# Performance work log

Measured on AMD Instinct MI355X. Metric: run time of the kernel, lower is better.

The kernel has to match this reference:

```python
import jax, jax.numpy as jnp
import numpy as np

OUT_C, IN_C, KS, KN = 256, 256, 3, 4
TEMP = 1.0
D1 = OUT_C * KS            # 768
D2 = IN_C * KS             # 768
D2R = D2 // 2 + 1          # 385 (rfft width)


def _freq_indices():
    # mirror torch get_fft2freq(d1, d2, use_rfft=True)
    fh = np.fft.fftfreq(D1)
    fw = np.fft.rfftfreq(D2)
    grid = np.stack(np.meshgrid(fh, fw, indexing='ij'), axis=-1)  # (D1, D2R, 2)
    dist = np.linalg.norm(grid, axis=-1).ravel()
    idx = np.argsort(dist, kind='stable')
    return (idx // D2R).astype(np.int32), (idx % D2R).astype(np.int32)


def setup_inputs() -> dict:
    key = jax.random.key(0)
    k1, k2, k3 = jax.random.split(key, 3)
    b, h, w = 8, 64, 64
    fh, fw = _freq_indices()
    num_freq = fh.shape[0]  # 295680 = D1 * D2R (param_reduction == 1.0)
    return {
        'x': jax.random.normal(k1, (b, IN_C, h, w), dtype=jnp.float32),
        'dft_weight': jax.random.normal(k2, (KN, num_freq, 2), dtype=jnp.float32) * 1e-6,
        'k_att': jax.random.normal(k3, (b, KN, 1, 1), dtype=jnp.float32),
        'freq_h': jnp.asarray(fh),
        'freq_w': jnp.asarray(fw),
    }


def reference(x, dft_weight, k_att, freq_h, freq_w):
    b, c, h, w = x.shape
    # kernel attention: sigmoid(att / temp) * 2 / kernel_num
    att = jax.nn.sigmoid(k_att / TEMP) * (2.0 / KN)          # (b, KN, 1, 1)
    # weighted sum of per-kernel frequency weights -> (b, F, 2)
    wsum = jnp.einsum('knf,bk->bnf', dft_weight, att.reshape(b, KN))
    wc = jax.lax.complex(wsum[..., 0], wsum[..., 1])          # (b, F) complex
    # scatter into dense rfft2 map (indices are a permutation: no duplicates)
    dft_map = jnp.zeros((b, D1, D2R), dtype=jnp.complex64)
    dft_map = dft_map.at[:, freq_h, freq_w].set(wc)
    # inverse rFFT2 -> spatial weights (b, D1, D2)
    sw = jnp.fft.irfft2(dft_map, s=(D1, D2))
    # (b, out, ks, in, ks) -> (b, out, in, ks, ks) -> grouped-conv kernel
    wk = sw.reshape(b, OUT_C, KS, IN_C, KS).transpose(0, 1, 3, 2, 4)
    wk = wk.reshape(b * OUT_C, IN_C, KS, KS)
    # batch of per-sample convs == one grouped conv with groups=b
    xg = x.reshape(1, b * c, h, w)
    out = jax.lax.conv_general_dilated(
        xg, wk, window_strides=(1, 1), padding=[(1, 1), (1, 1)],
        dimension_numbers=('NCHW', 'OIHW', 'NCHW'), feature_group_count=b)
    return out.reshape(b, OUT_C, out.shape[2], out.shape[3])
```

## Files before the change

### kernel.cpp

```cpp
#include <hip/hip_runtime.h>
#include <math.h>

#define D1 768
#define D2R 385
#define NF 295680
#define KNUM 4
#define NB 8
#define NC 256
#define TWOPI_768 0.008181230868723419f
#define INV768 0.0013020833333333333f

#define ATW_U32 1572864u
#define YA_U32 2752512u
#define T_U32 3981312u
#define SPECB_K_U32 344064u
#define WBF_BYTE 9437184u

typedef __attribute__((ext_vector_type(8))) short short8;
typedef __attribute__((ext_vector_type(16))) float f32x16;
typedef __attribute__((ext_vector_type(4))) float f4;
union U4S8 { unsigned int u[4]; uint4 u4; short8 s8; };

static __device__ __forceinline__ unsigned int f2bf(float f) {
  unsigned int u = __float_as_uint(f);
  return (u + 0x7fffu + ((u >> 16) & 1u)) >> 16;
}

static __device__ __forceinline__ void sincos_rev768(int idx, float* s,
                                                     float* c) {
  float rev = (float)idx * INV768;
  *s = __builtin_amdgcn_sinf(rev);
  *c = __builtin_amdgcn_cosf(rev);
}

static __device__ __forceinline__ void barrier_lgkm() {
  asm volatile("s_waitcnt lgkmcnt(0)" ::: "memory");
  __builtin_amdgcn_sched_barrier(0);
  __builtin_amdgcn_s_barrier();
  __builtin_amdgcn_sched_barrier(0);
}

__global__ __launch_bounds__(256) void prep_kernel(
    const float* __restrict__ dw, const int* __restrict__ fh,
    const int* __restrict__ fw, unsigned int* __restrict__ ws) {
  long i = (long)blockIdx.x * 256 + threadIdx.x;
  if (i < 1182720) {
    int k = (int)(i / NF);
    int r = (int)(i - (long)k * NF);
    const float2 v = ((const float2*)dw)[i];
    int h = fh[r], c = fw[r];
    ws[(size_t)k * SPECB_K_U32 + (size_t)c * 768 + h] =
        f2bf(v.x) | (f2bf(v.y) << 16);
    return;
  }
  long j = i - 1182720;
  if (j < 1179648) {
    int ri = (int)(j / 589824);
    int rem = (int)(j - (long)ri * 589824);
    int m = rem / 768, h = rem - (rem / 768) * 768;
    int idx = (h * m) % 768;
    float s, c;
    sincos_rev768(idx, &s, &c);
    unsigned lo, hi;
    if (ri == 0) { lo = f2bf(c); hi = f2bf(-s); }
    else         { lo = f2bf(s); hi = f2bf(c); }
    ws[ATW_U32 + j] = lo | (hi << 16);
  } else if (j < 1486848) {
    long p = j - 1179648;
    int n = (int)(p / 400), cc = (int)(p - (p / 400) * 400);
    unsigned v = 0;
    if (cc <= 384) {
      float wgt = (cc == 0 || cc == 384) ? 1.6954210069444445e-6f
                                         : 3.390842013888889e-6f;
      int idx = (cc * n) % 768;
      float s, c;
      sincos_rev768(idx, &s, &c);
      v = f2bf(wgt * c) | (f2bf(-wgt * s) << 16);
    }
    ws[T_U32 + (size_t)n * 400 + cc] = v;
  } else if (j < 1680384) {
    long p = j - 1486848;
    int k = (int)(p / 48384);
    long r = p - (long)k * 48384;
    int row = 385 + (int)(r / 768);
    int col = (int)(r - (r / 768) * 768);
    ws[(size_t)k * SPECB_K_U32 + (size_t)row * 768 + col] = 0u;
  } else if (j < 1726464) {
    long p = j - 1680384;
    int k = (int)(p / 11520);
    long r = p - (long)k * 11520;
    int m = (int)(r / 15), jj = (int)(r - (r / 15) * 15);
    ws[YA_U32 + (size_t)k * 307200 + (size_t)m * 400 + 385 + jj] = 0u;
  }
}

__global__ __launch_bounds__(256) void fftA_kernel(
    const unsigned short* __restrict__ Atw,
    const unsigned short* __restrict__ specB,
    unsigned short* __restrict__ Ya) {
  __shared__ __align__(16) unsigned short Al[2][64 * 40], Bl[2][64 * 40];
  int t = threadIdx.x;
  int mt = blockIdx.x, nt = blockIdx.y, z = blockIdx.z;
  int ri = z & 1, k = z >> 1;
  const unsigned short* Ag =
      Atw + (size_t)ri * 1179648 + (size_t)(mt * 64) * 1536;
  const unsigned short* Bg =
      specB + (size_t)k * 688128 + (size_t)(nt * 64) * 1536;
  int rowS = t >> 2, q = t & 3;
  int lane = t & 63, w = t >> 6;
  int moff = (w & 1) * 32, noff = (w >> 1) * 32;
  int lm = lane & 31, half = lane >> 5;
  int wr = rowS * 40 + q * 8;
  int ao = (moff + lm) * 40 + half * 8;
  int bo = (noff + lm) * 40 + half * 8;

  f32x16 acc;
#pragma unroll
  for (int r = 0; r < 16; ++r) acc[r] = 0.f;

  uint4 av = *(const uint4*)(Ag + (size_t)rowS * 1536 + q * 8);
  uint4 bv = *(const uint4*)(Bg + (size_t)rowS * 1536 + q * 8);
  *(uint4*)&Al[0][wr] = av;
  *(uint4*)&Bl[0][wr] = bv;
  __syncthreads();

  for (int kb = 0; kb < 48; ++kb) {
    bool more = (kb < 47);
    if (more) {
      av = *(const uint4*)(Ag + (size_t)rowS * 1536 + (kb + 1) * 32 + q * 8);
      bv = *(const uint4*)(Bg + (size_t)rowS * 1536 + (kb + 1) * 32 + q * 8);
    }
    const unsigned short* Ab = Al[kb & 1];
    const unsigned short* Bb = Bl[kb & 1];
#pragma unroll
    for (int kk2 = 0; kk2 < 2; ++kk2) {
      short8 a8 = *(const short8*)&Ab[ao + kk2 * 16];
      short8 b8 = *(const short8*)&Bb[bo + kk2 * 16];
      acc = __builtin_amdgcn_mfma_f32_32x32x16_bf16(a8, b8, acc, 0, 0, 0);
    }
    if (more) {
      *(uint4*)&Al[(kb + 1) & 1][wr] = av;
      *(uint4*)&Bl[(kb + 1) & 1][wr] = bv;
    }
    __syncthreads();
  }

  int c = nt * 64 + noff + lm;
  if (c < D2R) {
    unsigned short* Yk = Ya + (size_t)k * 614400;
    int mb = mt * 64 + moff + 4 * half;
#pragma unroll
    for (int reg = 0; reg < 16; ++reg) {
      int m = mb + (reg & 3) + 8 * (reg >> 2);
      Yk[(size_t)m * 800 + 2 * c + ri] = (unsigned short)f2bf(acc[reg]);
    }
  }
}

__global__ __launch_bounds__(256) void fftB_kernel(
    const unsigned short* __restrict__ Ya, const unsigned short* __restrict__ T,
    float* __restrict__ SW) {
  __shared__ __align__(16) unsigned short Al[2][64 * 40], Bl[2][64 * 40];
  int t = threadIdx.x;
  int mt = blockIdx.x, nt = blockIdx.y, k = blockIdx.z;
  const unsigned short* Ag = Ya + (size_t)k * 614400 + (size_t)(mt * 64) * 800;
  const unsigned short* Bg = T + (size_t)(nt * 64) * 800;
  int rowS = t >> 2, q = t & 3;
  int lane = t & 63, w = t >> 6;
  int moff = (w & 1) * 32, noff = (w >> 1) * 32;
  int lm = lane & 31, half = lane >> 5;
  int wr = rowS * 40 + q * 8;
  int ao = (moff + lm) * 40 + half * 8;
  int bo = (noff + lm) * 40 + half * 8;

  f32x16 acc;
#pragma unroll
  for (int r = 0; r < 16; ++r) acc[r] = 0.f;

  uint4 av = *(const uint4*)(Ag + (size_t)rowS * 800 + q * 8);
  uint4 bv = *(const uint4*)(Bg + (size_t)rowS * 800 + q * 8);
  *(uint4*)&Al[0][wr] = av;
  *(uint4*)&Bl[0][wr] = bv;
  __syncthreads();

  for (int kb = 0; kb < 25; ++kb) {
    bool more = (kb < 24);
    if (more) {
      av = *(const uint4*)(Ag + (size_t)rowS * 800 + (kb + 1) * 32 + q * 8);
      bv = *(const uint4*)(Bg + (size_t)rowS * 800 + (kb + 1) * 32 + q * 8);
    }
    const unsigned short* Ab = Al[kb & 1];
    const unsigned short* Bb = Bl[kb & 1];
#pragma unroll
    for (int kk2 = 0; kk2 < 2; ++kk2) {
      short8 a8 = *(const short8*)&Ab[ao + kk2 * 16];
      short8 b8 = *(const short8*)&Bb[bo + kk2 * 16];
      acc = __builtin_amdgcn_mfma_f32_32x32x16_bf16(a8, b8, acc, 0, 0, 0);
    }
    if (more) {
      *(uint4*)&Al[(kb + 1) & 1][wr] = av;
      *(uint4*)&Bl[(kb + 1) & 1][wr] = bv;
    }
    __syncthreads();
  }

  float* SWk = SW + (size_t)k * 589824;
  int n = nt * 64 + noff + lm;
  int mb = mt * 64 + moff + 4 * half;
#pragma unroll
  for (int reg = 0; reg < 16; ++reg) {
    int m = mb + (reg & 3) + 8 * (reg >> 2);
    SWk[(size_t)m * 768 + n] = acc[reg];
  }
}

__global__ __launch_bounds__(256) void wprep_kernel(
    const float* __restrict__ ka, const float* __restrict__ SW,
    unsigned short* __restrict__ wBF) {
  __shared__ float rowL[4][768];
  int t = threadIdx.x;
  int row = blockIdx.x;
  int oc = row / 3, dy = row - oc * 3;
  if (t < 192) {
#pragma unroll
    for (int k = 0; k < 4; ++k)
      *(float4*)&rowL[k][t * 4] =
          *(const float4*)(SW + (size_t)k * 589824 + (size_t)row * 768 + t * 4);
  }
  float att[8][4];
#pragma unroll
  for (int b = 0; b < 8; ++b)
#pragma unroll
    for (int k = 0; k < 4; ++k)
      att[b][k] = 0.5f / (1.f + expf(-ka[b * 4 + k]));
  __syncthreads();
  int icb = t >> 4, i = t & 15;
#pragma unroll
  for (int dx = 0; dx < 3; ++dx) {
    int col = icb * 48 + dx + 3 * i;
    float v0 = rowL[0][col], v1 = rowL[1][col], v2 = rowL[2][col],
          v3 = rowL[3][col];
    int s = dy * 3 + dx;
#pragma unroll
    for (int b = 0; b < 8; ++b) {
      float v = att[b][0] * v0 + att[b][1] * v1 + att[b][2] * v2 +
                att[b][3] * v3;
      wBF[(((size_t)(b * 16 + icb) * 9 + s) * 256 + oc) * 16 + i] =
          (unsigned short)f2bf(v);
    }
  }
}

static __device__ __forceinline__ void stage_write(unsigned char* xw, f4 v0,
                                                   f4 v1, f4 v2, f4 v3) {
#pragma unroll
  for (int pp = 0; pp < 4; ++pp) {
    uint2 wv;
    wv.x = f2bf(v0[pp]) | (f2bf(v1[pp]) << 16);
    wv.y = f2bf(v2[pp]) | (f2bf(v3[pp]) << 16);
    *(uint2*)(xw + pp * 48) = wv;
  }
}

__global__ __launch_bounds__(256, 2) void conv_mfma_kernel(
    const float* __restrict__ x, const unsigned short* __restrict__ wBF,
    float* __restrict__ out) {
  __shared__ __align__(16) unsigned char ldsX[2][4 * 66 * 48];
  int t = threadIdx.x;
  int pxt = blockIdx.x, oct = blockIdx.y, b = blockIdx.z;
  int py0 = pxt * 2, oc0 = oct * 128;
  int lane = t & 63, w = t >> 6;
  int ocq = w >> 1, pxq = w & 1;
  int n = lane & 31, half = lane >> 5;

  if (t < 192) {
    int buf = t / 96, r2 = t - buf * 96;
    int site = r2 / 12, word = r2 - site * 12;
    int r = site >> 1, c = (site & 1) ? 65 : 0;
    *(unsigned int*)(&ldsX[buf][(r * 66 + c) * 48 + word * 4]) = 0u;
  }

  f32x16 acc[2][2];
#pragma unroll
  for (int i = 0; i < 2; ++i)
#pragma unroll
    for (int j = 0; j < 2; ++j)
#pragma unroll
      for (int r = 0; r < 16; ++r) acc[i][j][r] = 0.f;

  int px4 = lane & 15, sub = lane >> 4;
  int iy = py0 - 1 + sub;
  bool valid = (iy >= 0 && iy < 64);
  const float* xpb =
      x + (((size_t)(b * NC + w * 4)) * 64 + (valid ? iy : 0)) * 64 + px4 * 4;
  int xwbase = (sub * 66 + 1 + px4 * 4) * 48 + w * 8;

  f4 a0 = {0.f, 0.f, 0.f, 0.f}, a1 = a0, a2 = a0, a3 = a0;
  if (valid) {
    const float* p0 = xpb;
    a0 = *(const f4*)(p0);
    a1 = *(const f4*)(p0 + 4096);
    a2 = *(const f4*)(p0 + 8192);
    a3 = *(const f4*)(p0 + 12288);
  }

  const uint4* wg4 = (const uint4*)wBF;
  size_t abase =
      (size_t)b * 144 * 512 + (size_t)(oc0 + ocq * 64 + n) * 2 + half;
  U4S8 pf[9][2];
#pragma unroll
  for (int i = 0; i < 9; ++i) {
    pf[i][0].u4 = wg4[abase + (size_t)i * 512];
    pf[i][1].u4 = wg4[abase + (size_t)i * 512 + 64];
  }

  stage_write(&ldsX[0][0] + xwbase, a0, a1, a2, a3);
  barrier_lgkm();

  for (int icb = 0; icb < 16; ++icb) {
    a0 = a1 = a2 = a3 = (f4){0.f, 0.f, 0.f, 0.f};
    if (icb < 15 && valid) {
      const float* p0 = xpb + (size_t)(icb + 1) * 16 * 4096;
      a0 = *(const f4*)(p0);
      a1 = *(const f4*)(p0 + 4096);
      a2 = *(const f4*)(p0 + 8192);
      a3 = *(const f4*)(p0 + 12288);
    }
    const unsigned char* bufR = &ldsX[icb & 1][0];
#pragma unroll
    for (int s = 0; s < 9; ++s) {
      int step = icb * 9 + s;
      int dy = s / 3, dx = s - dy * 3;
      const unsigned char* bb =
          bufR + ((pxq + dy) * 66 + n + dx) * 48 + half * 16;
      short8 B0 = *(const short8*)bb;
      short8 B1 = *(const short8*)(bb + 32 * 48);
      acc[0][0] = __builtin_amdgcn_mfma_f32_32x32x16_bf16(pf[s][0].s8, B0,
                                                          acc[0][0], 0, 0, 0);
      acc[0][1] = __builtin_amdgcn_mfma_f32_32x32x16_bf16(pf[s][0].s8, B1,
                                                          acc[0][1], 0, 0, 0);
      acc[1][0] = __builtin_amdgcn_mfma_f32_32x32x16_bf16(pf[s][1].s8, B0,
                                                          acc[1][0], 0, 0, 0);
      acc[1][1] = __builtin_amdgcn_mfma_f32_32x32x16_bf16(pf[s][1].s8, B1,
                                                          acc[1][1], 0, 0, 0);
      if (icb < 15) {
        pf[s][0].u4 = wg4[abase + (size_t)(step + 9) * 512];
        pf[s][1].u4 = wg4[abase + (size_t)(step + 9) * 512 + 64];
      }
    }
    if (icb < 15)
      stage_write(&ldsX[(icb + 1) & 1][0] + xwbase, a0, a1, a2, a3);
    barrier_lgkm();
  }

  int py = py0 + pxq;
#pragma unroll
  for (int osub = 0; osub < 2; ++osub)
#pragma unroll
    for (int psub = 0; psub < 2; ++psub) {
      int OC = oc0 + ocq * 64 + osub * 32 + 4 * half;
      int pxc = psub * 32 + n;
      float* op = out + (((size_t)(b * NC + OC)) * 64 + py) * 64 + pxc;
#pragma unroll
      for (int reg = 0; reg < 16; ++reg) {
        int ocm = (reg & 3) + 8 * (reg >> 2);
        op[(size_t)ocm * 4096] = acc[osub][psub][reg];
      }
    }
}

extern "C" void kernel_launch(void* const* d_in, const int* in_sizes, int n_in,
                              void* d_out, int out_size, void* d_ws,
                              size_t ws_size, hipStream_t stream) {
  const float* x = (const float*)d_in[0];
  const float* dw = (const float*)d_in[1];
  const float* ka = (const float*)d_in[2];
  const int* fh = (const int*)d_in[3];
  const int* fw = (const int*)d_in[4];
  float* out = (float*)d_out;
  unsigned int* ws = (unsigned int*)d_ws;
  const unsigned short* specB = (const unsigned short*)d_ws;
  const unsigned short* Atw = (const unsigned short*)((char*)d_ws + 6291456);
  unsigned short* Ya = (unsigned short*)((char*)d_ws + 11010048);
  const unsigned short* T = (const unsigned short*)((char*)d_ws + 15925248);
  float* SW = (float*)d_ws;
  unsigned short* wBF = (unsigned short*)((char*)d_ws + WBF_BYTE);

  hipLaunchKernelGGL(prep_kernel, dim3(11364), dim3(256), 0, stream, dw, fh,
                     fw, ws);
  hipLaunchKernelGGL(fftA_kernel, dim3(12, 7, 8), dim3(256), 0, stream, Atw,
                     specB, Ya);
  hipLaunchKernelGGL(fftB_kernel, dim3(12, 12, KNUM), dim3(256), 0, stream, Ya,
                     T, SW);
  hipLaunchKernelGGL(wprep_kernel, dim3(768), dim3(256), 0, stream, ka, SW,
                     wBF);
  hipLaunchKernelGGL(conv_mfma_kernel, dim3(32, 2, NB), dim3(256), 0, stream,
                     x, wBF, out);
}
```

Before: 192.7 us.

## Enlarge FFT GEMM M-tiles, remap conv blocks per XCD, shrink conv LDS stride

The two DFT GEMM kernels now compute 128x64 tiles per block with two accumulators per wave, so each B fragment read from LDS feeds two MFMAs and half as many blocks are launched. The conv kernel is launched on a 1D grid and remaps block IDs so that blocks sharing a batch and output-channel slice land on the same XCD, which should improve L2 reuse of weights and input. The conv input staging changes to a strided pixel assignment with a 40-byte LDS row stride instead of 48, reducing LDS footprint and changing the bank pattern, at the cost of scalar global loads instead of float4. The larger GEMM tiles reduce block-level parallelism for the small FFT GEMMs and raise register pressure.

```diff
diff --git a/kernel.cpp b/kernel.cpp
--- a/kernel.cpp
+++ b/kernel.cpp
@@ -18,7 +18,6 @@
 
 typedef __attribute__((ext_vector_type(8))) short short8;
 typedef __attribute__((ext_vector_type(16))) float f32x16;
-typedef __attribute__((ext_vector_type(4))) float f4;
 union U4S8 { unsigned int u[4]; uint4 u4; short8 s8; };
 
 static __device__ __forceinline__ unsigned int f2bf(float f) {
@@ -98,61 +97,75 @@
     const unsigned short* __restrict__ Atw,
     const unsigned short* __restrict__ specB,
     unsigned short* __restrict__ Ya) {
-  __shared__ __align__(16) unsigned short Al[2][64 * 40], Bl[2][64 * 40];
+  __shared__ __align__(16) unsigned short Al[2][128 * 40], Bl[2][64 * 40];
   int t = threadIdx.x;
   int mt = blockIdx.x, nt = blockIdx.y, z = blockIdx.z;
   int ri = z & 1, k = z >> 1;
   const unsigned short* Ag =
-      Atw + (size_t)ri * 1179648 + (size_t)(mt * 64) * 1536;
+      Atw + (size_t)ri * 1179648 + (size_t)(mt * 128) * 1536;
   const unsigned short* Bg =
       specB + (size_t)k * 688128 + (size_t)(nt * 64) * 1536;
-  int rowS = t >> 2, q = t & 3;
+  int rowA = t >> 1, qa = t & 1;
+  int rowB = t >> 2, qb = t & 3;
   int lane = t & 63, w = t >> 6;
-  int moff = (w & 1) * 32, noff = (w >> 1) * 32;
+  int mq = w & 1, nq = w >> 1;
   int lm = lane & 31, half = lane >> 5;
-  int wr = rowS * 40 + q * 8;
-  int ao = (moff + lm) * 40 + half * 8;
-  int bo = (noff + lm) * 40 + half * 8;
-
-  f32x16 acc;
-#pragma unroll
-  for (int r = 0; r < 16; ++r) acc[r] = 0.f;
-
-  uint4 av = *(const uint4*)(Ag + (size_t)rowS * 1536 + q * 8);
-  uint4 bv = *(const uint4*)(Bg + (size_t)rowS * 1536 + q * 8);
-  *(uint4*)&Al[0][wr] = av;
-  *(uint4*)&Bl[0][wr] = bv;
+  int wrA = rowA * 40 + qa * 16;
+  int wrB = rowB * 40 + qb * 8;
+  int ao0 = (mq * 64 + lm) * 40 + half * 8;
+  int ao1 = (mq * 64 + 32 + lm) * 40 + half * 8;
+  int bo = (nq * 32 + lm) * 40 + half * 8;
+
+  f32x16 acc[2];
+#pragma unroll
+  for (int i = 0; i < 2; ++i)
+#pragma unroll
+    for (int r = 0; r < 16; ++r) acc[i][r] = 0.f;
+
+  uint4 av0 = *(const uint4*)(Ag + (size_t)rowA * 1536 + qa * 16);
+  uint4 av1 = *(const uint4*)(Ag + (size_t)rowA * 1536 + qa * 16 + 8);
+  uint4 bv = *(const uint4*)(Bg + (size_t)rowB * 1536 + qb * 8);
+  *(uint4*)&Al[0][wrA] = av0;
+  *(uint4*)&Al[0][wrA + 8] = av1;
+  *(uint4*)&Bl[0][wrB] = bv;
   __syncthreads();
 
   for (int kb = 0; kb < 48; ++kb) {
     bool more = (kb < 47);
     if (more) {
-      av = *(const uint4*)(Ag + (size_t)rowS * 1536 + (kb + 1) * 32 + q * 8);
-      bv = *(const uint4*)(Bg + (size_t)rowS * 1536 + (kb + 1) * 32 + q * 8);
+      av0 = *(const uint4*)(Ag + (size_t)rowA * 1536 + (kb + 1) * 32 + qa * 16);
+      av1 = *(const uint4*)(Ag + (size_t)rowA * 1536 + (kb + 1) * 32 + qa * 16 + 8);
+      bv = *(const uint4*)(Bg + (size_t)rowB * 1536 + (kb + 1) * 32 + qb * 8);
     }
     const unsigned short* Ab = Al[kb & 1];
     const unsigned short* Bb = Bl[kb & 1];
 #pragma unroll
     for (int kk2 = 0; kk2 < 2; ++kk2) {
-      short8 a8 = *(const short8*)&Ab[ao + kk2 * 16];
       short8 b8 = *(const short8*)&Bb[bo + kk2 * 16];
-      acc = __builtin_amdgcn_mfma_f32_32x32x16_bf16(a8, b8, acc, 0, 0, 0);
+      short8 a80 = *(const short8*)&Ab[ao0 + kk2 * 16];
+      short8 a81 = *(const short8*)&Ab[ao1 + kk2 * 16];
+      acc[0] = __builtin_amdgcn_mfma_f32_32x32x16_bf16(a80, b8, acc[0], 0, 0, 0);
+      acc[1] = __builtin_amdgcn_mfma_f32_32x32x16_bf16(a81, b8, acc[1], 0, 0, 0);
     }
     if (more) {
-      *(uint4*)&Al[(kb + 1) & 1][wr] = av;
-      *(uint4*)&Bl[(kb + 1) & 1][wr] = bv;
+      *(uint4*)&Al[(kb + 1) & 1][wrA] = av0;
+      *(uint4*)&Al[(kb + 1) & 1][wrA + 8] = av1;
+      *(uint4*)&Bl[(kb + 1) & 1][wrB] = bv;
     }
     __syncthreads();
   }
 
-  int c = nt * 64 + noff + lm;
+  int c = nt * 64 + nq * 32 + lm;
   if (c < D2R) {
     unsigned short* Yk = Ya + (size_t)k * 614400;
-    int mb = mt * 64 + moff + 4 * half;
-#pragma unroll
-    for (int reg = 0; reg < 16; ++reg) {
-      int m = mb + (reg & 3) + 8 * (reg >> 2);
-      Yk[(size_t)m * 800 + 2 * c + ri] = (unsigned short)f2bf(acc[reg]);
+#pragma unroll
+    for (int i = 0; i < 2; ++i) {
+      int mb = mt * 128 + mq * 64 + i * 32 + 4 * half;
+#pragma unroll
+      for (int reg = 0; reg < 16; ++reg) {
+        int m = mb + (reg & 3) + 8 * (reg >> 2);
+        Yk[(size_t)m * 800 + 2 * c + ri] = (unsigned short)f2bf(acc[i][reg]);
+      }
     }
   }
 }
@@ -160,57 +173,71 @@
 __global__ __launch_bounds__(256) void fftB_kernel(
     const unsigned short* __restrict__ Ya, const unsigned short* __restrict__ T,
     float* __restrict__ SW) {
-  __shared__ __align__(16) unsigned short Al[2][64 * 40], Bl[2][64 * 40];
+  __shared__ __align__(16) unsigned short Al[2][128 * 40], Bl[2][64 * 40];
   int t = threadIdx.x;
   int mt = blockIdx.x, nt = blockIdx.y, k = blockIdx.z;
-  const unsigned short* Ag = Ya + (size_t)k * 614400 + (size_t)(mt * 64) * 800;
+  const unsigned short* Ag = Ya + (size_t)k * 614400 + (size_t)(mt * 128) * 800;
   const unsigned short* Bg = T + (size_t)(nt * 64) * 800;
-  int rowS = t >> 2, q = t & 3;
+  int rowA = t >> 1, qa = t & 1;
+  int rowB = t >> 2, qb = t & 3;
   int lane = t & 63, w = t >> 6;
-  int moff = (w & 1) * 32, noff = (w >> 1) * 32;
+  int mq = w & 1, nq = w >> 1;
   int lm = lane & 31, half = lane >> 5;
-  int wr = rowS * 40 + q * 8;
-  int ao = (moff + lm) * 40 + half * 8;
-  int bo = (noff + lm) * 40 + half * 8;
-
-  f32x16 acc;
-#pragma unroll
-  for (int r = 0; r < 16; ++r) acc[r] = 0.f;
-
-  uint4 av = *(const uint4*)(Ag + (size_t)rowS * 800 + q * 8);
-  uint4 bv = *(const uint4*)(Bg + (size_t)rowS * 800 + q * 8);
-  *(uint4*)&Al[0][wr] = av;
-  *(uint4*)&Bl[0][wr] = bv;
+  int wrA = rowA * 40 + qa * 16;
+  int wrB = rowB * 40 + qb * 8;
+  int ao0 = (mq * 64 + lm) * 40 + half * 8;
+  int ao1 = (mq * 64 + 32 + lm) * 40 + half * 8;
+  int bo = (nq * 32 + lm) * 40 + half * 8;
+
+  f32x16 acc[2];
+#pragma unroll
+  for (int i = 0; i < 2; ++i)
+#pragma unroll
+    for (int r = 0; r < 16; ++r) acc[i][r] = 0.f;
+
+  uint4 av0 = *(const uint4*)(Ag + (size_t)rowA * 800 + qa * 16);
+  uint4 av1 = *(const uint4*)(Ag + (size_t)rowA * 800 + qa * 16 + 8);
+  uint4 bv = *(const uint4*)(Bg + (size_t)rowB * 800 + qb * 8);
+  *(uint4*)&Al[0][wrA] = av0;
+  *(uint4*)&Al[0][wrA + 8] = av1;
+  *(uint4*)&Bl[0][wrB] = bv;
   __syncthreads();
 
   for (int kb = 0; kb < 25; ++kb) {
     bool more = (kb < 24);
     if (more) {
-      av = *(const uint4*)(Ag + (size_t)rowS * 800 + (kb + 1) * 32 + q * 8);
-      bv = *(const uint4*)(Bg + (size_t)rowS * 800 + (kb + 1) * 32 + q * 8);
+      av0 = *(const uint4*)(Ag + (size_t)rowA * 800 + (kb + 1) * 32 + qa * 16);
+      av1 = *(const uint4*)(Ag + (size_t)rowA * 800 + (kb + 1) * 32 + qa * 16 + 8);
+      bv = *(const uint4*)(Bg + (size_t)rowB * 800 + (kb + 1) * 32 + qb * 8);
     }
     const unsigned short* Ab = Al[kb & 1];
     const unsigned short* Bb = Bl[kb & 1];
 #pragma unroll
     for (int kk2 = 0; kk2 < 2; ++kk2) {
-      short8 a8 = *(const short8*)&Ab[ao + kk2 * 16];
       short8 b8 = *(const short8*)&Bb[bo + kk2 * 16];
-      acc = __builtin_amdgcn_mfma_f32_32x32x16_bf16(a8, b8, acc, 0, 0, 0);
+      short8 a80 = *(const short8*)&Ab[ao0 + kk2 * 16];
+      short8 a81 = *(const short8*)&Ab[ao1 + kk2 * 16];
+      acc[0] = __builtin_amdgcn_mfma_f32_32x32x16_bf16(a80, b8, acc[0], 0, 0, 0);
+      acc[1] = __builtin_amdgcn_mfma_f32_32x32x16_bf16(a81, b8, acc[1], 0, 0, 0);
     }
     if (more) {
-      *(uint4*)&Al[(kb + 1) & 1][wr] = av;
-      *(uint4*)&Bl[(kb + 1) & 1][wr] = bv;
+      *(uint4*)&Al[(kb + 1) & 1][wrA] = av0;
+      *(uint4*)&Al[(kb + 1) & 1][wrA + 8] = av1;
+      *(uint4*)&Bl[(kb + 1) & 1][wrB] = bv;
     }
     __syncthreads();
   }
 
   float* SWk = SW + (size_t)k * 589824;
-  int n = nt * 64 + noff + lm;
-  int mb = mt * 64 + moff + 4 * half;
-#pragma unroll
-  for (int reg = 0; reg < 16; ++reg) {
-    int m = mb + (reg & 3) + 8 * (reg >> 2);
-    SWk[(size_t)m * 768 + n] = acc[reg];
+  int n = nt * 64 + nq * 32 + lm;
+#pragma unroll
+  for (int i = 0; i < 2; ++i) {
+    int mb = mt * 128 + mq * 64 + i * 32 + 4 * half;
+#pragma unroll
+    for (int reg = 0; reg < 16; ++reg) {
+      int m = mb + (reg & 3) + 8 * (reg >> 2);
+      SWk[(size_t)m * 768 + n] = acc[i][reg];
+    }
   }
 }
 
@@ -251,33 +278,26 @@
   }
 }
 
-static __device__ __forceinline__ void stage_write(unsigned char* xw, f4 v0,
-                                                   f4 v1, f4 v2, f4 v3) {
-#pragma unroll
-  for (int pp = 0; pp < 4; ++pp) {
-    uint2 wv;
-    wv.x = f2bf(v0[pp]) | (f2bf(v1[pp]) << 16);
-    wv.y = f2bf(v2[pp]) | (f2bf(v3[pp]) << 16);
-    *(uint2*)(xw + pp * 48) = wv;
-  }
-}
-
 __global__ __launch_bounds__(256, 2) void conv_mfma_kernel(
     const float* __restrict__ x, const unsigned short* __restrict__ wBF,
     float* __restrict__ out) {
-  __shared__ __align__(16) unsigned char ldsX[2][4 * 66 * 48];
+  __shared__ __align__(16) unsigned char ldsX[2][4 * 66 * 40];
   int t = threadIdx.x;
-  int pxt = blockIdx.x, oct = blockIdx.y, b = blockIdx.z;
+  int orig = blockIdx.x;
+  int xcd = orig & 7, seq = orig >> 3;
+  int slice = xcd * 2 + (seq >> 5);
+  int pxt = seq & 31;
+  int b = slice >> 1, oct = slice & 1;
   int py0 = pxt * 2, oc0 = oct * 128;
   int lane = t & 63, w = t >> 6;
   int ocq = w >> 1, pxq = w & 1;
   int n = lane & 31, half = lane >> 5;
 
-  if (t < 192) {
-    int buf = t / 96, r2 = t - buf * 96;
-    int site = r2 / 12, word = r2 - site * 12;
+  if (t < 160) {
+    int buf = t / 80, r2 = t - buf * 80;
+    int site = r2 / 10, word = r2 - site * 10;
     int r = site >> 1, c = (site & 1) ? 65 : 0;
-    *(unsigned int*)(&ldsX[buf][(r * 66 + c) * 48 + word * 4]) = 0u;
+    *(unsigned int*)(&ldsX[buf][(r * 66 + c) * 40 + word * 4]) = 0u;
   }
 
   f32x16 acc[2][2];
@@ -292,16 +312,22 @@
   int iy = py0 - 1 + sub;
   bool valid = (iy >= 0 && iy < 64);
   const float* xpb =
-      x + (((size_t)(b * NC + w * 4)) * 64 + (valid ? iy : 0)) * 64 + px4 * 4;
-  int xwbase = (sub * 66 + 1 + px4 * 4) * 48 + w * 8;
-
-  f4 a0 = {0.f, 0.f, 0.f, 0.f}, a1 = a0, a2 = a0, a3 = a0;
+      x + (((size_t)(b * NC + w * 4)) * 64 + (valid ? iy : 0)) * 64 + px4;
+  unsigned char* xw0 = (unsigned char*)&ldsX[0][0] + (sub * 66 + 1 + px4) * 40 + w * 8;
+  unsigned char* xw1 = (unsigned char*)&ldsX[1][0] + (sub * 66 + 1 + px4) * 40 + w * 8;
+
+  float a[4][4];
+#pragma unroll
+  for (int j = 0; j < 4; ++j)
+#pragma unroll
+    for (int pp = 0; pp < 4; ++pp) a[j][pp] = 0.f;
   if (valid) {
-    const float* p0 = xpb;
-    a0 = *(const f4*)(p0);
-    a1 = *(const f4*)(p0 + 4096);
-    a2 = *(const f4*)(p0 + 8192);
-    a3 = *(const f4*)(p0 + 12288);
+#pragma unroll
+    for (int j = 0; j < 4; ++j) {
+      const float* pj = xpb + (size_t)j * 4096;
+#pragma unroll
+      for (int pp = 0; pp < 4; ++pp) a[j][pp] = pj[pp * 16];
+    }
   }
 
   const uint4* wg4 = (const uint4*)wBF;
@@ -314,17 +340,28 @@
     pf[i][1].u4 = wg4[abase + (size_t)i * 512 + 64];
   }
 
-  stage_write(&ldsX[0][0] + xwbase, a0, a1, a2, a3);
+#pragma unroll
+  for (int pp = 0; pp < 4; ++pp) {
+    uint2 wv;
+    wv.x = f2bf(a[0][pp]) | (f2bf(a[1][pp]) << 16);
+    wv.y = f2bf(a[2][pp]) | (f2bf(a[3][pp]) << 16);
+    *(uint2*)(xw0 + pp * 640) = wv;
+  }
   barrier_lgkm();
 
   for (int icb = 0; icb < 16; ++icb) {
-    a0 = a1 = a2 = a3 = (f4){0.f, 0.f, 0.f, 0.f};
+#pragma unroll
+    for (int j = 0; j < 4; ++j)
+#pragma unroll
+      for (int pp = 0; pp < 4; ++pp) a[j][pp] = 0.f;
     if (icb < 15 && valid) {
       const float* p0 = xpb + (size_t)(icb + 1) * 16 * 4096;
-      a0 = *(const f4*)(p0);
-      a1 = *(const f4*)(p0 + 4096);
-      a2 = *(const f4*)(p0 + 8192);
-      a3 = *(const f4*)(p0 + 12288);
+#pragma unroll
+      for (int j = 0; j < 4; ++j) {
+        const float* pj = p0 + (size_t)j * 4096;
+#pragma unroll
+        for (int pp = 0; pp < 4; ++pp) a[j][pp] = pj[pp * 16];
+      }
     }
     const unsigned char* bufR = &ldsX[icb & 1][0];
 #pragma unroll
@@ -332,9 +369,9 @@
       int step = icb * 9 + s;
       int dy = s / 3, dx = s - dy * 3;
       const unsigned char* bb =
-          bufR + ((pxq + dy) * 66 + n + dx) * 48 + half * 16;
+          bufR + ((pxq + dy) * 66 + n + dx) * 40 + half * 16;
       short8 B0 = *(const short8*)bb;
-      short8 B1 = *(const short8*)(bb + 32 * 48);
+      short8 B1 = *(const short8*)(bb + 32 * 40);
       acc[0][0] = __builtin_amdgcn_mfma_f32_32x32x16_bf16(pf[s][0].s8, B0,
                                                           acc[0][0], 0, 0, 0);
       acc[0][1] = __builtin_amdgcn_mfma_f32_32x32x16_bf16(pf[s][0].s8, B1,
@@ -348,8 +385,16 @@
         pf[s][1].u4 = wg4[abase + (size_t)(step + 9) * 512 + 64];
       }
     }
-    if (icb < 15)
-      stage_write(&ldsX[(icb + 1) & 1][0] + xwbase, a0, a1, a2, a3);
+    if (icb < 15) {
+      unsigned char* xw = (icb & 1) ? xw0 : xw1;
+#pragma unroll
+      for (int pp = 0; pp < 4; ++pp) {
+        uint2 wv;
+        wv.x = f2bf(a[0][pp]) | (f2bf(a[1][pp]) << 16);
+        wv.y = f2bf(a[2][pp]) | (f2bf(a[3][pp]) << 16);
+        *(uint2*)(xw + pp * 640) = wv;
+      }
+    }
     barrier_lgkm();
   }
 
@@ -388,12 +433,12 @@
 
   hipLaunchKernelGGL(prep_kernel, dim3(11364), dim3(256), 0, stream, dw, fh,
                      fw, ws);
-  hipLaunchKernelGGL(fftA_kernel, dim3(12, 7, 8), dim3(256), 0, stream, Atw,
+  hipLaunchKernelGGL(fftA_kernel, dim3(6, 7, 8), dim3(256), 0, stream, Atw,
                      specB, Ya);
-  hipLaunchKernelGGL(fftB_kernel, dim3(12, 12, KNUM), dim3(256), 0, stream, Ya,
+  hipLaunchKernelGGL(fftB_kernel, dim3(6, 12, KNUM), dim3(256), 0, stream, Ya,
                      T, SW);
   hipLaunchKernelGGL(wprep_kernel, dim3(768), dim3(256), 0, stream, ka, SW,
                      wBF);
-  hipLaunchKernelGGL(conv_mfma_kernel, dim3(32, 2, NB), dim3(256), 0, stream,
-                     x, wBF, out);
-}
+  hipLaunchKernelGGL(conv_mfma_kernel, dim3(512), dim3(256), 0, stream, x,
+                     wBF, out);
+}
```

Result: slower. 223.9 us (+16.2%).
